# Optimization experiments

Hardware: AMD Instinct MI355X
Metric: run time of the kernel (lower is better)

The kernel has to match this reference:

```python
import jax, jax.numpy as jnp
import numpy as np

B, S, D, DFF = 4, 2048, 1024, 4096


def setup_inputs() -> dict:
    key = jax.random.key(0)
    ks = jax.random.split(key, 7)
    scale = 1.0 / np.sqrt(D)
    return {
        "x": jax.random.normal(ks[0], (B, S, D), dtype=jnp.float32),
        "wq": jax.random.normal(ks[1], (D, D), dtype=jnp.float32) * scale,
        "wk": jax.random.normal(ks[2], (D, D), dtype=jnp.float32) * scale,
        "wv": jax.random.normal(ks[3], (D, D), dtype=jnp.float32) * scale,
        "wo": jax.random.normal(ks[4], (D, D), dtype=jnp.float32) * scale,
        "w1": jax.random.normal(ks[5], (D, DFF), dtype=jnp.float32) * scale,
        "w2": jax.random.normal(ks[6], (DFF, D), dtype=jnp.float32) * (1.0 / np.sqrt(DFF)),
    }


def reference(x, wq, wk, wv, wo, w1, w2):
    # Single-head attention, NO 1/sqrt(d) scaling (faithful to source).
    q = x @ wq  # [B,S,D]
    k = x @ wk
    v = x @ wv
    scores = jnp.einsum("bsd,btd->bst", q, k)  # [B,S,S]
    weights = jax.nn.softmax(scores, axis=-1)
    attn = jnp.einsum("bst,btd->bsd", weights, v)
    proj = attn @ wo
    hidden = jax.nn.relu(proj @ w1)  # [B,S,DFF]
    out = hidden @ w2
    return out + x
```

## Files before the change

kernel.cpp:

```cpp
#include <hip/hip_runtime.h>
#include <hip/hip_bf16.h>
#include <hip/hip_fp16.h>


typedef _Float16 f16;
typedef __attribute__((ext_vector_type(8))) _Float16 f16x8;
typedef __attribute__((ext_vector_type(4))) _Float16 f16x4;
typedef __attribute__((ext_vector_type(4))) float f32x4;

#define BM 128
#define BN 128
#define BK 64

__device__ inline void gload16(const void* g, void* l) {
    __builtin_amdgcn_global_load_lds(
        (const __attribute__((address_space(1))) void*)g,
        (__attribute__((address_space(3))) void*)l, 16, 0, 0);
}

template<int EPI>
__global__ __launch_bounds__(256, 2)
void gemm_f16(const f16* __restrict__ A, const f16* __restrict__ Bt,
              const float* __restrict__ Res, void* __restrict__ Cv,
              int K, int lda, int ldb, int ldc,
              long long sA, long long sB, long long sC)
{
    __shared__ char smem[32 * 1024];
    f16* Ash = (f16*)smem;
    f16* Bsh = (f16*)(smem + 16384);
    float* xbuf = (float*)smem;

    const int t = threadIdx.x;
    const int z = blockIdx.z;
    A  += (size_t)z * sA;
    Bt += (size_t)z * sB;

    const int bm0 = blockIdx.x * BM;
    const int bn0 = blockIdx.y * BN;

    const int lane = t & 63;
    const int wid  = t >> 6;
    const int quad = lane >> 4;
    const int m16  = lane & 15;
    const int ks   = wid & 1;
    const int wn64 = (wid >> 1) * 64;

    const int r0 = t >> 3;
    const int kc = ((t & 7) ^ (r0 & 7)) * 8;
    const char* gA[4]; const char* gB[4];
    #pragma unroll
    for (int i = 0; i < 4; ++i) {
        gA[i] = (const char*)(A  + (size_t)(bm0 + i * 32 + r0) * lda + kc);
        gB[i] = (const char*)(Bt + (size_t)(bn0 + i * 32 + r0) * ldb + kc);
    }
    char* lA = (char*)Ash + (wid << 10);
    char* lB = (char*)Bsh + (wid << 10);

    f32x4 acc[8][4] = {};

    const int nk = K / BK;
    #define ISSUE(kt) do { const int ko = (kt) * 128;   \
        gload16(gA[0] + ko, lA);                        \
        gload16(gA[1] + ko, lA + 4096);                 \
        gload16(gA[2] + ko, lA + 8192);                 \
        gload16(gA[3] + ko, lA + 12288);                \
        gload16(gB[0] + ko, lB);                        \
        gload16(gB[1] + ko, lB + 4096);                 \
        gload16(gB[2] + ko, lB + 8192);                 \
        gload16(gB[3] + ko, lB + 12288); } while (0)

    const int swz = m16 & 7;
    const int ha  = ((ks * 4 + quad) ^ swz) * 8;

    ISSUE(0);
    for (int kt = 0; kt < nk; ++kt) {
        __syncthreads();
        f16x8 af[8], bf[4];
        #pragma unroll
        for (int i = 0; i < 8; ++i)
            af[i] = *(const f16x8*)&Ash[(i * 16 + m16) * BK + ha];
        #pragma unroll
        for (int j = 0; j < 4; ++j)
            bf[j] = *(const f16x8*)&Bsh[(wn64 + j * 16 + m16) * BK + ha];
        __syncthreads();
        if (kt + 1 < nk) ISSUE(kt + 1);
        #pragma unroll
        for (int i = 0; i < 8; ++i)
            #pragma unroll
            for (int j = 0; j < 4; ++j)
                acc[i][j] = __builtin_amdgcn_mfma_f32_16x16x32_f16(
                                af[i], bf[j], acc[i][j], 0, 0, 0);
    }
    #undef ISSUE

    float* xb = xbuf + (wid >> 1) * 4096;
    #define XIDX(row, col) ((row) * 64 + ((col) ^ (((row) & 4) << 2)))
    if (ks == 1) {
        #pragma unroll
        for (int i = 0; i < 4; ++i)
            #pragma unroll
            for (int j = 0; j < 4; ++j)
                #pragma unroll
                for (int ri = 0; ri < 4; ++ri)
                    xb[XIDX(i * 16 + quad * 4 + ri, j * 16 + m16)] = acc[i][j][ri];
    }
    __syncthreads();
    if (ks == 0) {
        #pragma unroll
        for (int i = 0; i < 4; ++i)
            #pragma unroll
            for (int j = 0; j < 4; ++j)
                #pragma unroll
                for (int ri = 0; ri < 4; ++ri)
                    acc[i][j][ri] += xb[XIDX(i * 16 + quad * 4 + ri, j * 16 + m16)];
    }
    __syncthreads();
    if (ks == 0) {
        #pragma unroll
        for (int i = 0; i < 4; ++i)
            #pragma unroll
            for (int j = 0; j < 4; ++j)
                #pragma unroll
                for (int ri = 0; ri < 4; ++ri)
                    xb[XIDX(i * 16 + quad * 4 + ri, j * 16 + m16)] = acc[i + 4][j][ri];
    }
    __syncthreads();
    if (ks == 1) {
        #pragma unroll
        for (int i = 0; i < 4; ++i)
            #pragma unroll
            for (int j = 0; j < 4; ++j)
                #pragma unroll
                for (int ri = 0; ri < 4; ++ri)
                    acc[i + 4][j][ri] += xb[XIDX(i * 16 + quad * 4 + ri, j * 16 + m16)];
    }
    #undef XIDX

    #define STORE_TILE(IB, RB)                                                  \
        do {                                                                    \
            float* C = (float*)Cv + (size_t)z * sC;                             \
            _Pragma("unroll")                                                   \
            for (int i = 0; i < 4; ++i)                                         \
                _Pragma("unroll")                                               \
                for (int ri = 0; ri < 4; ++ri) {                                \
                    const size_t row = (size_t)(bm0 + (RB) + i * 16 + quad * 4 + ri); \
                    float* cp = C + row * ldc + (bn0 + wn64 + m16);             \
                    const float* rp = Res + row * ldc + (bn0 + wn64 + m16);     \
                    _Pragma("unroll")                                           \
                    for (int j = 0; j < 4; ++j) {                               \
                        float v = acc[(IB) + i][j][ri];                         \
                        if (EPI == 3) v += rp[j * 16];                          \
                        cp[j * 16] = v;                                         \
                    }                                                           \
                }                                                               \
        } while (0)

    if (ks == 0) STORE_TILE(0, 0);
    else         STORE_TILE(4, 64);
    #undef STORE_TILE
}

template<int EPI>
__global__ __launch_bounds__(256, 2)
void gemm_ns2(const f16* __restrict__ A, const f16* __restrict__ Bt,
              void* __restrict__ Cv,
              int K, int lda, int ldb, int ldc,
              long long sA, long long sB, long long sC)
{
    __shared__ f16 Ash[BM * BK];
    __shared__ f16 Bsh[BN * BK];

    const int t = threadIdx.x;
    const int z = blockIdx.z;
    A  += (size_t)z * sA;
    Bt += (size_t)z * sB;

    const int bm0 = blockIdx.x * BM;
    const int bn0 = blockIdx.y * BN;

    const int lane = t & 63;
    const int wid  = t >> 6;
    const int quad = lane >> 4;
    const int m16  = lane & 15;
    const int wm = (wid & 1) * 64;
    const int wn = (wid >> 1) * 64;

    const int r0 = t >> 3;
    const int kc = ((t & 7) ^ (r0 & 7)) * 8;
    const char* gA[4]; const char* gB[4];
    #pragma unroll
    for (int i = 0; i < 4; ++i) {
        gA[i] = (const char*)(A  + (size_t)(bm0 + i * 32 + r0) * lda + kc);
        gB[i] = (const char*)(Bt + (size_t)(bn0 + i * 32 + r0) * ldb + kc);
    }
    char* lA = (char*)Ash + (wid << 10);
    char* lB = (char*)Bsh + (wid << 10);

    f32x4 acc[4][4] = {};

    const int nk = K / BK;
    #define ISSUE(kt) do { const int ko = (kt) * 128;   \
        gload16(gA[0] + ko, lA);                        \
        gload16(gA[1] + ko, lA + 4096);                 \
        gload16(gA[2] + ko, lA + 8192);                 \
        gload16(gA[3] + ko, lA + 12288);                \
        gload16(gB[0] + ko, lB);                        \
        gload16(gB[1] + ko, lB + 4096);                 \
        gload16(gB[2] + ko, lB + 8192);                 \
        gload16(gB[3] + ko, lB + 12288); } while (0)

    const int swz = m16 & 7;

    ISSUE(0);
    for (int kt = 0; kt < nk; ++kt) {
        __syncthreads();
        f16x8 af[2][4], bf[2][4];
        #pragma unroll
        for (int s = 0; s < 2; ++s) {
            const int ha = (((s << 2) | quad) ^ swz) * 8;
            #pragma unroll
            for (int i = 0; i < 4; ++i) {
                af[s][i] = *(const f16x8*)&Ash[(wm + i * 16 + m16) * BK + ha];
                bf[s][i] = *(const f16x8*)&Bsh[(wn + i * 16 + m16) * BK + ha];
            }
        }
        __syncthreads();
        if (kt + 1 < nk) ISSUE(kt + 1);
        #pragma unroll
        for (int s = 0; s < 2; ++s)
            #pragma unroll
            for (int i = 0; i < 4; ++i)
                #pragma unroll
                for (int j = 0; j < 4; ++j)
                    acc[i][j] = __builtin_amdgcn_mfma_f32_16x16x32_f16(
                                    af[s][i], bf[s][j], acc[i][j], 0, 0, 0);
    }
    #undef ISSUE

    if (EPI <= 1) {
        f16* C = (f16*)Cv + (size_t)z * sC;
        #pragma unroll
        for (int i = 0; i < 4; ++i)
            #pragma unroll
            for (int ri = 0; ri < 4; ++ri) {
                const size_t row = (size_t)(bm0 + wm + i * 16 + quad * 4 + ri);
                f16* cp = C + row * ldc + (bn0 + wn + m16);
                #pragma unroll
                for (int j = 0; j < 4; ++j) {
                    float v = acc[i][j][ri];
                    if (EPI == 1) v = fmaxf(v, 0.0f);
                    cp[j * 16] = (f16)v;
                }
            }
    } else {
        float* C = (float*)Cv + (size_t)z * sC;
        #pragma unroll
        for (int i = 0; i < 4; ++i)
            #pragma unroll
            for (int ri = 0; ri < 4; ++ri) {
                const size_t row = (size_t)(bm0 + wm + i * 16 + quad * 4 + ri);
                float* cp = C + row * ldc + (bn0 + wn + m16);
                #pragma unroll
                for (int j = 0; j < 4; ++j)
                    cp[j * 16] = acc[i][j][ri];
            }
    }
}

__global__ __launch_bounds__(256, 2)
void gemm_dd(const f16* __restrict__ A0, const f16* __restrict__ B0, f16* __restrict__ C0,
             const f16* __restrict__ A1, const f16* __restrict__ B1, f16* __restrict__ C1)
{
    const int LD = 1024;
    __shared__ char smem[32 * 1024];
    f16* Ash = (f16*)smem;
    f16* Bsh = (f16*)(smem + 16384);
    float* xred = (float*)smem;

    const int t = threadIdx.x;
    const int z = blockIdx.z;
    const f16* A = z ? A1 : A0;
    const f16* B = z ? B1 : B0;
    f16* C = z ? C1 : C0;

    const int bm0 = blockIdx.x * 64;
    const int bn0 = blockIdx.y * 64;

    const int lane = t & 63;
    const int wid  = t >> 6;
    const int quad = lane >> 4;
    const int m16  = lane & 15;

    const int rr = t >> 4;
    const int kc = ((t & 15) ^ (rr & 15)) * 8;
    const char* gA[4]; const char* gB[4];
    #pragma unroll
    for (int i = 0; i < 4; ++i) {
        gA[i] = (const char*)(A + (size_t)(bm0 + i * 16 + rr) * LD + kc);
        gB[i] = (const char*)(B + (size_t)(bn0 + i * 16 + rr) * LD + kc);
    }
    char* lA = (char*)Ash + (wid << 10);
    char* lB = (char*)Bsh + (wid << 10);

    f32x4 acc[4][4] = {};

    #define ISSUE(kt) do { const int ko = (kt) * 256;   \
        gload16(gA[0] + ko, lA);                        \
        gload16(gA[1] + ko, lA + 4096);                 \
        gload16(gA[2] + ko, lA + 8192);                 \
        gload16(gA[3] + ko, lA + 12288);                \
        gload16(gB[0] + ko, lB);                        \
        gload16(gB[1] + ko, lB + 4096);                 \
        gload16(gB[2] + ko, lB + 8192);                 \
        gload16(gB[3] + ko, lB + 12288); } while (0)

    const int sl = ((wid * 4 + quad) ^ m16) * 8;

    ISSUE(0);
    for (int kt = 0; kt < 8; ++kt) {
        __syncthreads();
        f16x8 af[4], bf[4];
        #pragma unroll
        for (int i = 0; i < 4; ++i) {
            af[i] = *(const f16x8*)&Ash[(i * 16 + m16) * 128 + sl];
            bf[i] = *(const f16x8*)&Bsh[(i * 16 + m16) * 128 + sl];
        }
        __syncthreads();
        if (kt + 1 < 8) ISSUE(kt + 1);
        #pragma unroll
        for (int i = 0; i < 4; ++i)
            #pragma unroll
            for (int j = 0; j < 4; ++j)
                acc[i][j] = __builtin_amdgcn_mfma_f32_16x16x32_f16(
                                af[i], bf[j], acc[i][j], 0, 0, 0);
    }
    #undef ISSUE

    #define XIDX(row, col) ((row) * 64 + ((col) ^ (((row) & 4) << 2)))
    #define WR(base) do {                                                       \
        _Pragma("unroll")                                                       \
        for (int i = 0; i < 4; ++i)                                             \
            _Pragma("unroll")                                                   \
            for (int j = 0; j < 4; ++j)                                         \
                _Pragma("unroll")                                               \
                for (int ri = 0; ri < 4; ++ri)                                  \
                    (base)[XIDX(i * 16 + quad * 4 + ri, j * 16 + m16)] = acc[i][j][ri]; \
        } while (0)
    #define RD(base) do {                                                       \
        _Pragma("unroll")                                                       \
        for (int i = 0; i < 4; ++i)                                             \
            _Pragma("unroll")                                                   \
            for (int j = 0; j < 4; ++j)                                         \
                _Pragma("unroll")                                               \
                for (int ri = 0; ri < 4; ++ri)                                  \
                    acc[i][j][ri] += (base)[XIDX(i * 16 + quad * 4 + ri, j * 16 + m16)]; \
        } while (0)

    __syncthreads();
    if (wid == 2) WR(xred);
    if (wid == 3) WR(xred + 4096);
    __syncthreads();
    if (wid == 0) RD(xred);
    if (wid == 1) RD(xred + 4096);
    __syncthreads();
    if (wid == 1) WR(xred);
    __syncthreads();
    if (wid == 0) {
        RD(xred);
        #pragma unroll
        for (int i = 0; i < 4; ++i)
            #pragma unroll
            for (int ri = 0; ri < 4; ++ri) {
                const size_t row = (size_t)(bm0 + i * 16 + quad * 4 + ri);
                f16* cp = C + row * LD + (bn0 + m16);
                #pragma unroll
                for (int j = 0; j < 4; ++j)
                    cp[j * 16] = (f16)acc[i][j][ri];
            }
    }
    #undef WR
    #undef RD
    #undef XIDX
}

__global__ __launch_bounds__(256)
void transpose_all(const float* __restrict__ wo, const float* __restrict__ w1,
                   const float* __restrict__ w2,
                   f16* __restrict__ woT, f16* __restrict__ w1T,
                   f16* __restrict__ w2T)
{
    const int z = blockIdx.z;
    const float* in; f16* out; int R, C, gx, gy;
    if (z == 0)      { in = wo; out = woT; R = 1024; C = 1024; gx = 16; gy = 16; }
    else if (z == 1) { in = w1; out = w1T; R = 1024; C = 4096; gx = 64; gy = 16; }
    else             { in = w2; out = w2T; R = 4096; C = 1024; gx = 16; gy = 64; }
    if (blockIdx.x >= (unsigned)gx || blockIdx.y >= (unsigned)gy) return;

    __shared__ float tile[64][65];
    const int c0 = blockIdx.x * 64, r0 = blockIdx.y * 64;
    const int tc = threadIdx.x & 63, tr = threadIdx.x >> 6;
    #pragma unroll
    for (int i = 0; i < 16; ++i)
        tile[tr + i * 4][tc] = in[(size_t)(r0 + tr + i * 4) * C + c0 + tc];
    __syncthreads();
    #pragma unroll
    for (int i = 0; i < 16; ++i)
        out[(size_t)(c0 + tr + i * 4) * R + r0 + tc] = (f16)tile[tc][tr + i * 4];
}

__global__ __launch_bounds__(256)
void cast_all(const float* __restrict__ x, const float* __restrict__ wq,
              const float* __restrict__ wk, const float* __restrict__ wv,
              f16* __restrict__ xh, f16* __restrict__ wqh,
              f16* __restrict__ wkh, f16* __restrict__ wvh)
{
    const int z = blockIdx.z;
    const float* in; f16* out; unsigned nblk;
    if (z == 0)      { in = x;  out = xh;  nblk = 8192; }
    else if (z == 1) { in = wq; out = wqh; nblk = 1024; }
    else if (z == 2) { in = wk; out = wkh; nblk = 1024; }
    else             { in = wv; out = wvh; nblk = 1024; }
    if (blockIdx.x >= nblk) return;
    const size_t i = ((size_t)blockIdx.x * 256 + threadIdx.x) * 4;
    float4 v = *(const float4*)(in + i);
    f16x4 o; o.x = (f16)v.x; o.y = (f16)v.y; o.z = (f16)v.z; o.w = (f16)v.w;
    *(f16x4*)(out + i) = o;
}

__global__ __launch_bounds__(256)
void softmax_f16(float* __restrict__ S)
{
    __shared__ float red[256];
    float* p = S + (size_t)blockIdx.x * 2048;
    f16* q = (f16*)p;
    const int t = threadIdx.x;

    float4 u0 = *(const float4*)(p + t * 4);
    float4 u1 = *(const float4*)(p + 1024 + t * 4);

    float m = fmaxf(fmaxf(fmaxf(u0.x, u0.y), fmaxf(u0.z, u0.w)),
                    fmaxf(fmaxf(u1.x, u1.y), fmaxf(u1.z, u1.w)));
    red[t] = m;
    __syncthreads();
    #pragma unroll
    for (int s = 128; s > 0; s >>= 1) {
        if (t < s) red[t] = fmaxf(red[t], red[t + s]);
        __syncthreads();
    }
    const float rowmax = red[0];
    __syncthreads();

    u0.x = __expf(u0.x - rowmax); u0.y = __expf(u0.y - rowmax);
    u0.z = __expf(u0.z - rowmax); u0.w = __expf(u0.w - rowmax);
    u1.x = __expf(u1.x - rowmax); u1.y = __expf(u1.y - rowmax);
    u1.z = __expf(u1.z - rowmax); u1.w = __expf(u1.w - rowmax);

    red[t] = (u0.x + u0.y + u0.z + u0.w) + (u1.x + u1.y + u1.z + u1.w);
    __syncthreads();
    #pragma unroll
    for (int s = 128; s > 0; s >>= 1) {
        if (t < s) red[t] += red[t + s];
        __syncthreads();
    }
    const float inv = 1.0f / red[0];
    __syncthreads();

    f16x4 o0, o1;
    o0.x = (f16)(u0.x * inv); o0.y = (f16)(u0.y * inv);
    o0.z = (f16)(u0.z * inv); o0.w = (f16)(u0.w * inv);
    o1.x = (f16)(u1.x * inv); o1.y = (f16)(u1.y * inv);
    o1.z = (f16)(u1.z * inv); o1.w = (f16)(u1.w * inv);
    *(f16x4*)(q + t * 4)        = o0;
    *(f16x4*)(q + 1024 + t * 4) = o1;
}

extern "C" void kernel_launch(void* const* d_in, const int* in_sizes, int n_in,
                              void* d_out, int out_size, void* d_ws, size_t ws_size,
                              hipStream_t stream)
{
    const float* x  = (const float*)d_in[0];
    const float* wq = (const float*)d_in[1];
    const float* wk = (const float*)d_in[2];
    const float* wv = (const float*)d_in[3];
    const float* wo = (const float*)d_in[4];
    const float* w1 = (const float*)d_in[5];
    const float* w2 = (const float*)d_in[6];
    float* out = (float*)d_out;

    const int S = 2048, D = 1024, DFF = 4096, Bb = 4;
    const int NTOK = Bb * S;
    const size_t M1 = 1024 * 1024;

    f16* W    = (f16*)d_ws;
    f16* xh   = W;
    f16* wqh  = W + 8 * M1;
    f16* wkh  = W + 9 * M1;
    f16* wvh  = W + 10 * M1;
    f16* woT  = W + 11 * M1;
    f16* w1T  = W + 12 * M1;
    f16* w2T  = W + 16 * M1;
    f16* wqkT = W + 20 * M1;
    f16* wvoT = W + 21 * M1;
    f16* qp   = W + 22 * M1;
    f16* vwT  = W + 30 * M1;
    float* sb = (float*)(W + 38 * M1);
    f16* ph   = (f16*)sb;
    f16* pj   = xh;
    f16* hd   = qp;

    dim3 blk(256);

    cast_all<<<dim3(NTOK * D / 1024, 1, 4), blk, 0, stream>>>(
        x, wq, wk, wv, xh, wqh, wkh, wvh);
    transpose_all<<<dim3(64, 64, 3), blk, 0, stream>>>(
        wo, w1, w2, woT, w1T, w2T);
    gemm_dd<<<dim3(16, 16, 2), blk, 0, stream>>>(
        wkh, wqh, wqkT, woT, wvh, wvoT);

    gemm_ns2<0><<<dim3(NTOK / BM, D / BN, 1), blk, 0, stream>>>(
        xh, wqkT, qp, D, D, D, D, 0, 0, 0);
    gemm_ns2<0><<<dim3(D / BM, NTOK / BN, 1), blk, 0, stream>>>(
        wvoT, xh, vwT, D, D, D, NTOK, 0, 0, 0);

    gemm_ns2<2><<<dim3(S / BM, S / BN, Bb), blk, 0, stream>>>(
        qp, xh, sb, D, D, D, S,
        (long long)S * D, (long long)S * D, (long long)S * S);

    softmax_f16<<<dim3(NTOK), blk, 0, stream>>>(sb);

    gemm_ns2<0><<<dim3(S / BM, D / BN, Bb), blk, 0, stream>>>(
        ph, vwT, pj, S, 4096, NTOK, D,
        (long long)S * 4096, (long long)S, (long long)S * D);

    gemm_ns2<1><<<dim3(NTOK / BM, DFF / BN, 1), blk, 0, stream>>>(
        pj, w1T, hd, D, D, D, DFF, 0, 0, 0);

    gemm_f16<3><<<dim3(NTOK / BM, D / BN, 1), blk, 0, stream>>>(
        hd, w2T, x, out, DFF, DFF, DFF, D, 0, 0, 0);
}
```

Measured before the change: 421.2 us.

## Unify GEMM kernels, raise occupancy, split k-slice loads, use wave-shuffle softmax

Drops the split-K gemm_f16 kernel, which reduced partial sums across waves through LDS, and routes the final residual GEMM through gemm_ns2 with an added residual epilogue. The GEMM launch bounds go from 2 to 4 waves-per-EU occupancy, and the inner loop now loads and issues MFMAs for the first k-half before loading the second, so fewer fragments are live at once. Softmax reductions change from LDS tree reductions with many barriers to wave shuffles plus a 4-entry LDS combine. The higher occupancy bound risks register spilling, and the final GEMM loses the split-K parallelism it had before.

```diff
diff --git a/kernel.cpp b/kernel.cpp
--- a/kernel.cpp
+++ b/kernel.cpp
@@ -19,16 +19,14 @@
 }
 
 template<int EPI>
-__global__ __launch_bounds__(256, 2)
-void gemm_f16(const f16* __restrict__ A, const f16* __restrict__ Bt,
+__global__ __launch_bounds__(256, 4)
+void gemm_ns2(const f16* __restrict__ A, const f16* __restrict__ Bt,
               const float* __restrict__ Res, void* __restrict__ Cv,
               int K, int lda, int ldb, int ldc,
               long long sA, long long sB, long long sC)
 {
-    __shared__ char smem[32 * 1024];
-    f16* Ash = (f16*)smem;
-    f16* Bsh = (f16*)(smem + 16384);
-    float* xbuf = (float*)smem;
+    __shared__ f16 Ash[BM * BK];
+    __shared__ f16 Bsh[BN * BK];
 
     const int t = threadIdx.x;
     const int z = blockIdx.z;
@@ -42,8 +40,8 @@
     const int wid  = t >> 6;
     const int quad = lane >> 4;
     const int m16  = lane & 15;
-    const int ks   = wid & 1;
-    const int wn64 = (wid >> 1) * 64;
+    const int wm = (wid & 1) * 64;
+    const int wn = (wid >> 1) * 64;
 
     const int r0 = t >> 3;
     const int kc = ((t & 7) ^ (r0 & 7)) * 8;
@@ -56,7 +54,7 @@
     char* lA = (char*)Ash + (wid << 10);
     char* lB = (char*)Bsh + (wid << 10);
 
-    f32x4 acc[8][4] = {};
+    f32x4 acc[4][4] = {};
 
     const int nk = K / BK;
     #define ISSUE(kt) do { const int ko = (kt) * 128;   \
@@ -70,170 +68,37 @@
         gload16(gB[3] + ko, lB + 12288); } while (0)
 
     const int swz = m16 & 7;
-    const int ha  = ((ks * 4 + quad) ^ swz) * 8;
+    const int ha0 = ((quad)     ^ swz) * 8;
+    const int ha1 = ((4 | quad) ^ swz) * 8;
 
     ISSUE(0);
     for (int kt = 0; kt < nk; ++kt) {
         __syncthreads();
-        f16x8 af[8], bf[4];
-        #pragma unroll
-        for (int i = 0; i < 8; ++i)
-            af[i] = *(const f16x8*)&Ash[(i * 16 + m16) * BK + ha];
-        #pragma unroll
-        for (int j = 0; j < 4; ++j)
-            bf[j] = *(const f16x8*)&Bsh[(wn64 + j * 16 + m16) * BK + ha];
-        __syncthreads();
-        if (kt + 1 < nk) ISSUE(kt + 1);
-        #pragma unroll
-        for (int i = 0; i < 8; ++i)
+        f16x8 af[4], bf[4];
+        #pragma unroll
+        for (int i = 0; i < 4; ++i) {
+            af[i] = *(const f16x8*)&Ash[(wm + i * 16 + m16) * BK + ha0];
+            bf[i] = *(const f16x8*)&Bsh[(wn + i * 16 + m16) * BK + ha0];
+        }
+        #pragma unroll
+        for (int i = 0; i < 4; ++i)
             #pragma unroll
             for (int j = 0; j < 4; ++j)
                 acc[i][j] = __builtin_amdgcn_mfma_f32_16x16x32_f16(
                                 af[i], bf[j], acc[i][j], 0, 0, 0);
-    }
-    #undef ISSUE
-
-    float* xb = xbuf + (wid >> 1) * 4096;
-    #define XIDX(row, col) ((row) * 64 + ((col) ^ (((row) & 4) << 2)))
-    if (ks == 1) {
-        #pragma unroll
-        for (int i = 0; i < 4; ++i)
-            #pragma unroll
-            for (int j = 0; j < 4; ++j)
-                #pragma unroll
-                for (int ri = 0; ri < 4; ++ri)
-                    xb[XIDX(i * 16 + quad * 4 + ri, j * 16 + m16)] = acc[i][j][ri];
-    }
-    __syncthreads();
-    if (ks == 0) {
-        #pragma unroll
-        for (int i = 0; i < 4; ++i)
-            #pragma unroll
-            for (int j = 0; j < 4; ++j)
-                #pragma unroll
-                for (int ri = 0; ri < 4; ++ri)
-                    acc[i][j][ri] += xb[XIDX(i * 16 + quad * 4 + ri, j * 16 + m16)];
-    }
-    __syncthreads();
-    if (ks == 0) {
-        #pragma unroll
-        for (int i = 0; i < 4; ++i)
-            #pragma unroll
-            for (int j = 0; j < 4; ++j)
-                #pragma unroll
-                for (int ri = 0; ri < 4; ++ri)
-                    xb[XIDX(i * 16 + quad * 4 + ri, j * 16 + m16)] = acc[i + 4][j][ri];
-    }
-    __syncthreads();
-    if (ks == 1) {
-        #pragma unroll
-        for (int i = 0; i < 4; ++i)
-            #pragma unroll
-            for (int j = 0; j < 4; ++j)
-                #pragma unroll
-                for (int ri = 0; ri < 4; ++ri)
-                    acc[i + 4][j][ri] += xb[XIDX(i * 16 + quad * 4 + ri, j * 16 + m16)];
-    }
-    #undef XIDX
-
-    #define STORE_TILE(IB, RB)                                                  \
-        do {                                                                    \
-            float* C = (float*)Cv + (size_t)z * sC;                             \
-            _Pragma("unroll")                                                   \
-            for (int i = 0; i < 4; ++i)                                         \
-                _Pragma("unroll")                                               \
-                for (int ri = 0; ri < 4; ++ri) {                                \
-                    const size_t row = (size_t)(bm0 + (RB) + i * 16 + quad * 4 + ri); \
-                    float* cp = C + row * ldc + (bn0 + wn64 + m16);             \
-                    const float* rp = Res + row * ldc + (bn0 + wn64 + m16);     \
-                    _Pragma("unroll")                                           \
-                    for (int j = 0; j < 4; ++j) {                               \
-                        float v = acc[(IB) + i][j][ri];                         \
-                        if (EPI == 3) v += rp[j * 16];                          \
-                        cp[j * 16] = v;                                         \
-                    }                                                           \
-                }                                                               \
-        } while (0)
-
-    if (ks == 0) STORE_TILE(0, 0);
-    else         STORE_TILE(4, 64);
-    #undef STORE_TILE
-}
-
-template<int EPI>
-__global__ __launch_bounds__(256, 2)
-void gemm_ns2(const f16* __restrict__ A, const f16* __restrict__ Bt,
-              void* __restrict__ Cv,
-              int K, int lda, int ldb, int ldc,
-              long long sA, long long sB, long long sC)
-{
-    __shared__ f16 Ash[BM * BK];
-    __shared__ f16 Bsh[BN * BK];
-
-    const int t = threadIdx.x;
-    const int z = blockIdx.z;
-    A  += (size_t)z * sA;
-    Bt += (size_t)z * sB;
-
-    const int bm0 = blockIdx.x * BM;
-    const int bn0 = blockIdx.y * BN;
-
-    const int lane = t & 63;
-    const int wid  = t >> 6;
-    const int quad = lane >> 4;
-    const int m16  = lane & 15;
-    const int wm = (wid & 1) * 64;
-    const int wn = (wid >> 1) * 64;
-
-    const int r0 = t >> 3;
-    const int kc = ((t & 7) ^ (r0 & 7)) * 8;
-    const char* gA[4]; const char* gB[4];
-    #pragma unroll
-    for (int i = 0; i < 4; ++i) {
-        gA[i] = (const char*)(A  + (size_t)(bm0 + i * 32 + r0) * lda + kc);
-        gB[i] = (const char*)(Bt + (size_t)(bn0 + i * 32 + r0) * ldb + kc);
-    }
-    char* lA = (char*)Ash + (wid << 10);
-    char* lB = (char*)Bsh + (wid << 10);
-
-    f32x4 acc[4][4] = {};
-
-    const int nk = K / BK;
-    #define ISSUE(kt) do { const int ko = (kt) * 128;   \
-        gload16(gA[0] + ko, lA);                        \
-        gload16(gA[1] + ko, lA + 4096);                 \
-        gload16(gA[2] + ko, lA + 8192);                 \
-        gload16(gA[3] + ko, lA + 12288);                \
-        gload16(gB[0] + ko, lB);                        \
-        gload16(gB[1] + ko, lB + 4096);                 \
-        gload16(gB[2] + ko, lB + 8192);                 \
-        gload16(gB[3] + ko, lB + 12288); } while (0)
-
-    const int swz = m16 & 7;
-
-    ISSUE(0);
-    for (int kt = 0; kt < nk; ++kt) {
-        __syncthreads();
-        f16x8 af[2][4], bf[2][4];
-        #pragma unroll
-        for (int s = 0; s < 2; ++s) {
-            const int ha = (((s << 2) | quad) ^ swz) * 8;
-            #pragma unroll
-            for (int i = 0; i < 4; ++i) {
-                af[s][i] = *(const f16x8*)&Ash[(wm + i * 16 + m16) * BK + ha];
-                bf[s][i] = *(const f16x8*)&Bsh[(wn + i * 16 + m16) * BK + ha];
-            }
+        #pragma unroll
+        for (int i = 0; i < 4; ++i) {
+            af[i] = *(const f16x8*)&Ash[(wm + i * 16 + m16) * BK + ha1];
+            bf[i] = *(const f16x8*)&Bsh[(wn + i * 16 + m16) * BK + ha1];
         }
         __syncthreads();
         if (kt + 1 < nk) ISSUE(kt + 1);
         #pragma unroll
-        for (int s = 0; s < 2; ++s)
-            #pragma unroll
-            for (int i = 0; i < 4; ++i)
-                #pragma unroll
-                for (int j = 0; j < 4; ++j)
-                    acc[i][j] = __builtin_amdgcn_mfma_f32_16x16x32_f16(
-                                    af[s][i], bf[s][j], acc[i][j], 0, 0, 0);
+        for (int i = 0; i < 4; ++i)
+            #pragma unroll
+            for (int j = 0; j < 4; ++j)
+                acc[i][j] = __builtin_amdgcn_mfma_f32_16x16x32_f16(
+                                af[i], bf[j], acc[i][j], 0, 0, 0);
     }
     #undef ISSUE
 
@@ -260,9 +125,14 @@
             for (int ri = 0; ri < 4; ++ri) {
                 const size_t row = (size_t)(bm0 + wm + i * 16 + quad * 4 + ri);
                 float* cp = C + row * ldc + (bn0 + wn + m16);
+                const float* rp = (EPI == 3)
+                    ? Res + row * ldc + (bn0 + wn + m16) : nullptr;
                 #pragma unroll
-                for (int j = 0; j < 4; ++j)
-                    cp[j * 16] = acc[i][j][ri];
+                for (int j = 0; j < 4; ++j) {
+                    float v = acc[i][j][ri];
+                    if (EPI == 3) v += rp[j * 16];
+                    cp[j * 16] = v;
+                }
             }
     }
 }
@@ -430,40 +300,37 @@
 __global__ __launch_bounds__(256)
 void softmax_f16(float* __restrict__ S)
 {
-    __shared__ float red[256];
+    __shared__ float redm[4], reds[4];
     float* p = S + (size_t)blockIdx.x * 2048;
     f16* q = (f16*)p;
     const int t = threadIdx.x;
+    const int lane = t & 63, wid = t >> 6;
 
     float4 u0 = *(const float4*)(p + t * 4);
     float4 u1 = *(const float4*)(p + 1024 + t * 4);
 
     float m = fmaxf(fmaxf(fmaxf(u0.x, u0.y), fmaxf(u0.z, u0.w)),
                     fmaxf(fmaxf(u1.x, u1.y), fmaxf(u1.z, u1.w)));
-    red[t] = m;
-    __syncthreads();
-    #pragma unroll
-    for (int s = 128; s > 0; s >>= 1) {
-        if (t < s) red[t] = fmaxf(red[t], red[t + s]);
-        __syncthreads();
-    }
-    const float rowmax = red[0];
-    __syncthreads();
+    #pragma unroll
+    for (int off = 32; off > 0; off >>= 1)
+        m = fmaxf(m, __shfl_xor(m, off));
+    if (lane == 0) redm[wid] = m;
+    __syncthreads();
+    const float rowmax = fmaxf(fmaxf(redm[0], redm[1]),
+                               fmaxf(redm[2], redm[3]));
 
     u0.x = __expf(u0.x - rowmax); u0.y = __expf(u0.y - rowmax);
     u0.z = __expf(u0.z - rowmax); u0.w = __expf(u0.w - rowmax);
     u1.x = __expf(u1.x - rowmax); u1.y = __expf(u1.y - rowmax);
     u1.z = __expf(u1.z - rowmax); u1.w = __expf(u1.w - rowmax);
 
-    red[t] = (u0.x + u0.y + u0.z + u0.w) + (u1.x + u1.y + u1.z + u1.w);
-    __syncthreads();
-    #pragma unroll
-    for (int s = 128; s > 0; s >>= 1) {
-        if (t < s) red[t] += red[t + s];
-        __syncthreads();
-    }
-    const float inv = 1.0f / red[0];
-    __syncthreads();
+    float s = (u0.x + u0.y + u0.z + u0.w) + (u1.x + u1.y + u1.z + u1.w);
+    #pragma unroll
+    for (int off = 32; off > 0; off >>= 1)
+        s += __shfl_xor(s, off);
+    if (lane == 0) reds[wid] = s;
+    __syncthreads();
+    const float inv = 1.0f / (reds[0] + reds[1] + reds[2] + reds[3]);
 
     f16x4 o0, o1;
     o0.x = (f16)(u0.x * inv); o0.y = (f16)(u0.y * inv);
@@ -518,23 +385,23 @@
         wkh, wqh, wqkT, woT, wvh, wvoT);
 
     gemm_ns2<0><<<dim3(NTOK / BM, D / BN, 1), blk, 0, stream>>>(
-        xh, wqkT, qp, D, D, D, D, 0, 0, 0);
+        xh, wqkT, nullptr, qp, D, D, D, D, 0, 0, 0);
     gemm_ns2<0><<<dim3(D / BM, NTOK / BN, 1), blk, 0, stream>>>(
-        wvoT, xh, vwT, D, D, D, NTOK, 0, 0, 0);
+        wvoT, xh, nullptr, vwT, D, D, D, NTOK, 0, 0, 0);
 
     gemm_ns2<2><<<dim3(S / BM, S / BN, Bb), blk, 0, stream>>>(
-        qp, xh, sb, D, D, D, S,
+        qp, xh, nullptr, sb, D, D, D, S,
         (long long)S * D, (long long)S * D, (long long)S * S);
 
     softmax_f16<<<dim3(NTOK), blk, 0, stream>>>(sb);
 
     gemm_ns2<0><<<dim3(S / BM, D / BN, Bb), blk, 0, stream>>>(
-        ph, vwT, pj, S, 4096, NTOK, D,
+        ph, vwT, nullptr, pj, S, 4096, NTOK, D,
         (long long)S * 4096, (long long)S, (long long)S * D);
 
     gemm_ns2<1><<<dim3(NTOK / BM, DFF / BN, 1), blk, 0, stream>>>(
-        pj, w1T, hd, D, D, D, DFF, 0, 0, 0);
-
-    gemm_f16<3><<<dim3(NTOK / BM, D / BN, 1), blk, 0, stream>>>(
+        pj, w1T, nullptr, hd, D, D, D, DFF, 0, 0, 0);
+
+    gemm_ns2<3><<<dim3(NTOK / BM, D / BN, 1), blk, 0, stream>>>(
         hd, w2T, x, out, DFF, DFF, DFF, D, 0, 0, 0);
 }
```

After: 425.5 us. Within noise of the previous version (+1.0%).
